# Kernel tuning notes

Hardware: AMD Instinct MI355X
Metric: run time of the kernel (lower is better)

## Reference

```python
import jax, jax.numpy as jnp
import numpy as np

STRIDES = (8, 16, 32, 64, 128)
SIZES = ((40, 40), (20, 20), (10, 10), (5, 5), (3, 3))
NUM_CLASSES = 80
SCORE_THR = 0.025
NMS_PRE = 1000
IOU_THR = 0.5
IMG = 320.0  # img_shape hardcoded to (320, 320); clamp uses max_shape[1]
B = 4


def setup_inputs() -> dict:
    key = jax.random.key(0)
    ks = jax.random.split(key, 15)
    inp = {}
    for i, (h, w) in enumerate(SIZES):
        inp[f"cls{i}"] = jax.random.normal(ks[3 * i], (B, NUM_CLASSES, h, w), dtype=jnp.float32)
        # bbox preds are ltrb distances; scale uniform noise to plausible pixel distances
        inp[f"bbox{i}"] = jax.random.uniform(ks[3 * i + 1], (B, 4, h, w), dtype=jnp.float32) * 64.0
        inp[f"ctr{i}"] = jax.random.normal(ks[3 * i + 2], (B, 1, h, w), dtype=jnp.float32)
    return inp


def _priors(h, w, stride):
    # MlvlPointGenerator: (arange + 0.5) * stride, x fastest-varying
    sx = (jnp.arange(w, dtype=jnp.float32) + 0.5) * stride
    sy = (jnp.arange(h, dtype=jnp.float32) + 0.5) * stride
    return jnp.stack([jnp.tile(sx, h), jnp.repeat(sy, w)], axis=-1)  # [h*w, 2]


def _distance2bbox(points, dist):
    x1 = points[:, 0] - dist[:, 0]
    y1 = points[:, 1] - dist[:, 1]
    x2 = points[:, 0] + dist[:, 2]
    y2 = points[:, 1] + dist[:, 3]
    # torch.clamp_ on the whole tensor: min=0, max=max_shape[1]=320
    return jnp.clip(jnp.stack([x1, y1, x2, y2], axis=-1), 0.0, IMG)


def _pairwise_iou(boxes):
    # torchvision-style IoU on [K,4] boxes
    area = (boxes[:, 2] - boxes[:, 0]) * (boxes[:, 3] - boxes[:, 1])
    lt = jnp.maximum(boxes[:, None, :2], boxes[None, :, :2])
    rb = jnp.minimum(boxes[:, None, 2:], boxes[None, :, 2:])
    wh = jnp.maximum(rb - lt, 0.0)
    inter = wh[..., 0] * wh[..., 1]
    union = area[:, None] + area[None, :] - inter
    safe = jnp.where(union > 0.0, union, 1.0)
    return jnp.where(union > 0.0, inter / safe, 0.0)


def _single(cls_l, bbox_l, ctr_l):
    """Post-process one image. Returns fixed-size (dets [K,5], labels [K], keep [K] bool)."""
    scores_l, labels_l, boxes_l, valid_l = [], [], [], []
    for lvl in range(5):
        h, w = SIZES[lvl]
        pri = _priors(h, w, STRIDES[lvl])
        s = jax.nn.sigmoid(jnp.transpose(cls_l[lvl], (1, 2, 0)).reshape(-1, NUM_CLASSES)).reshape(-1)
        bp = jnp.transpose(bbox_l[lvl], (1, 2, 0)).reshape(-1, 4)
        sf = jax.nn.sigmoid(jnp.transpose(ctr_l[lvl], (1, 2, 0)).reshape(-1))
        # filter_scores_and_topk: mask scores <= thr to -1 so they sort last; fixed-size top_k
        k = min(NMS_PRE, s.shape[0])
        top_s, top_i = jax.lax.top_k(jnp.where(s > SCORE_THR, s, -1.0), k)
        anchor = top_i // NUM_CLASSES
        label = top_i % NUM_CLASSES
        valid = top_s > SCORE_THR
        boxes = _distance2bbox(pri[anchor], bp[anchor])
        # scores multiplied by centerness score factor (FCOS)
        scores_l.append(jnp.where(valid, top_s * sf[anchor], -1.0))
        labels_l.append(label)
        boxes_l.append(boxes)
        valid_l.append(valid)
    scores = jnp.concatenate(scores_l)          # [K]
    labels = jnp.concatenate(labels_l)          # [K]
    boxes = jnp.concatenate(boxes_l, axis=0)    # [K,4]
    valid = jnp.concatenate(valid_l)            # [K]
    # sort by final score descending (NMS processes in score order)
    order = jnp.argsort(-scores)
    scores = scores[order]
    labels = labels[order]
    boxes = boxes[order]
    valid = valid[order]
    # batched_nms: per-class coordinate offset trick
    max_coord = boxes.max()
    off = boxes + (labels.astype(jnp.float32) * (max_coord + 1.0))[:, None]
    iou = _pairwise_iou(off)  # [K,K]
    K = scores.shape[0]
    idx = jnp.arange(K)

    def body(i, keep):
        sup = (iou[i] > IOU_THR) & (idx > i) & keep[i]
        return keep & jnp.logical_not(sup)

    keep = jax.lax.fori_loop(0, K, body, valid)
    dets = jnp.concatenate([boxes, scores[:, None]], axis=-1)  # [K,5]
    return dets, labels, keep


def reference(cls0, cls1, cls2, cls3, cls4, bbox0, bbox1, bbox2, bbox3, bbox4, ctr0, ctr1, ctr2, ctr3, ctr4):
    cls_l = (cls0, cls1, cls2, cls3, cls4)
    bbox_l = (bbox0, bbox1, bbox2, bbox3, bbox4)
    ctr_l = (ctr0, ctr1, ctr2, ctr3, ctr4)
    return jax.vmap(_single)(cls_l, bbox_l, ctr_l)
```

## Files before the change

### kernel.cpp

```cpp
#include <hip/hip_runtime.h>
#include <stdint.h>


#define BN 4
#define NC 80
#define TOT 170720
#define KTOT 4720
#define NWIN 74
#define NJT 19
#define TIE_CAP 4096
#define IMGSZ 320.0f
#define PAIR_CAP 131072
#define LDSP 12288
#define SPC_CAP 4096

struct InPtrs {
  const float* cls[5];
  const float* bbox[5];
  const float* ctr[5];
};

__device__ __forceinline__ uint32_t f2s(float f) {
  uint32_t x = __float_as_uint(f);
  return (x & 0x80000000u) ? ~x : (x | 0x80000000u);
}
__device__ __forceinline__ float s2f(uint32_t s) {
  uint32_t x = (s & 0x80000000u) ? (s & 0x7fffffffu) : ~s;
  return __uint_as_float(x);
}
__device__ __forceinline__ float sigmoid32(float v) {
  float e = (float)exp(-(double)v);
  return __fdiv_rn(1.0f, __fadd_rn(1.0f, e));
}
__device__ __forceinline__ void lvl_of(int e, int& l, int& le) {
  if (e < 128000)      { l = 0; le = e; }
  else if (e < 160000) { l = 1; le = e - 128000; }
  else if (e < 168000) { l = 2; le = e - 160000; }
  else if (e < 170000) { l = 3; le = e - 168000; }
  else                 { l = 4; le = e - 170000; }
}
__device__ __forceinline__ int kl_of(int l) {
  constexpr int KL[5] = {1000, 1000, 1000, 1000, 720};
  return KL[l];
}
__device__ __forceinline__ float clip32(float v) {
  return fminf(fmaxf(v, 0.0f), IMGSZ);
}
__device__ __forceinline__ void tile_of(int t, int& l, int& p0) {
  if (t < 25)       { l = 0; p0 = t * 64; }
  else if (t < 32)  { l = 1; p0 = (t - 25) * 64; }
  else if (t < 34)  { l = 2; p0 = (t - 32) * 64; }
  else if (t == 34) { l = 3; p0 = 0; }
  else              { l = 4; p0 = 0; }
}
__device__ __forceinline__ int iou_gt(float bx1, float by1, float bx2, float by2,
                                      float bai, float4 o) {
  float ta_ = __fmul_rn(__fsub_rn(o.z, o.x), __fsub_rn(o.w, o.y));
  float ltx = fmaxf(bx1, o.x), lty = fmaxf(by1, o.y);
  float rbx = fminf(bx2, o.z), rby = fminf(by2, o.w);
  float wd = fmaxf(__fsub_rn(rbx, ltx), 0.0f);
  float hg = fmaxf(__fsub_rn(rby, lty), 0.0f);
  float inter = __fmul_rn(wd, hg);
  float asum = __fadd_rn(bai, ta_);
  float uni  = __fsub_rn(asum, inter);
  float iou  = (uni > 0.0f) ? __fdiv_rn(inter, uni) : 0.0f;
  return (iou > 0.5f) ? 1 : 0;
}

__global__ void k_score(InPtrs in, uint32_t* __restrict__ su, uint32_t* __restrict__ hist0) {
  int b = blockIdx.y;
  int tl, p0; tile_of(blockIdx.x, tl, p0);
  constexpr int HWc[5]  = {1600, 400, 100, 25, 9};
  constexpr int LOFF[5] = {0, 128000, 160000, 168000, 170000};
  int hw = HWc[tl];
  int tw = min(64, hw - p0);
  int tid = threadIdx.x;
  __shared__ uint32_t lu[64 * 81];
  __shared__ uint32_t lh[1024];
  for (int i = tid; i < 1024; i += 256) lh[i] = 0;
  __syncthreads();
  int pf = tid & 63;
  if (pf < tw) {
    const float* cp = in.cls[tl] + (size_t)b * NC * hw + p0 + pf;
    for (int c = tid >> 6; c < NC; c += 4) {
      float v = cp[(size_t)c * hw];
      float s = sigmoid32(v);
      float m = (s > 0.025f) ? s : -1.0f;
      uint32_t u = f2s(m);
      lu[pf * 81 + c] = u;
      atomicAdd(&lh[u >> 22], 1u);
    }
  }
  __syncthreads();
  int bl = b * 5 + tl;
  for (int i = tid; i < 1024; i += 256)
    if (lh[i]) atomicAdd(&hist0[(size_t)bl * 1024 + i], lh[i]);
  int n = tw * NC;
  uint32_t* dst = su + (size_t)b * TOT + LOFF[tl] + p0 * NC;
  for (int idx = tid; idx < n; idx += 256)
    dst[idx] = lu[(idx / 80) * 81 + (idx % 80)];
}

__global__ void k_scan1(const uint32_t* __restrict__ su, const uint32_t* __restrict__ mpfx,
                        uint32_t* __restrict__ hist1) {
  int b = blockIdx.y;
  int tid = threadIdx.x;
  int e0 = blockIdx.x * 256;
  int e = e0 + tid;
  int l0, le0; lvl_of(e0, l0, le0);
  __shared__ uint32_t lh[2][1024];
  for (int i = tid; i < 2048; i += 256) lh[i >> 10][i & 1023] = 0;
  __syncthreads();
  if (e < TOT) {
    int l, le; lvl_of(e, l, le);
    uint32_t C = mpfx[b * 5 + l];
    uint32_t u = su[(size_t)b * TOT + e];
    if ((u >> 22) == (C >> 22)) atomicAdd(&lh[l - l0][(u >> 12) & 1023u], 1u);
  }
  __syncthreads();
  for (int s = 0; s < 2; s++) {
    int l = l0 + s;
    if (l >= 5) break;
    int bl = b * 5 + l;
    for (int i = tid; i < 1024; i += 256)
      if (lh[s][i]) atomicAdd(&hist1[(size_t)bl * 1024 + i], lh[s][i]);
  }
}

__global__ void k_scan2(const uint32_t* __restrict__ su, const uint32_t* __restrict__ mpfx,
                        uint32_t* __restrict__ hist2) {
  int b = blockIdx.y;
  int e = blockIdx.x * blockDim.x + threadIdx.x;
  if (e >= TOT) return;
  int l, le; lvl_of(e, l, le);
  int bl = b * 5 + l;
  uint32_t C = mpfx[bl];
  uint32_t u = su[(size_t)b * TOT + e];
  if ((u >> 12) == (C >> 12))
    atomicAdd(&hist2[(size_t)bl * 4096 + (u & 4095u)], 1u);
}

__global__ void k_findp(const uint32_t* __restrict__ hist, uint32_t* __restrict__ mpfx,
                        uint32_t* __restrict__ mk, int nbins, int shift, int pass) {
  int bl = blockIdx.x;
  uint32_t k = (pass == 0) ? (uint32_t)kl_of(bl % 5) : mk[bl];
  const uint32_t* h = hist + (size_t)bl * nbins;
  __shared__ uint32_t gsum[256];
  int tid = threadIdx.x;
  int per = nbins / 256;
  int base = tid * per;
  uint32_t s = 0;
  for (int i = 0; i < per; i++) s += h[base + i];
  gsum[tid] = s;
  __syncthreads();
  uint32_t above = 0;
  for (int t = tid + 1; t < 256; t++) above += gsum[t];
  if (above < k && above + s >= k) {
    uint32_t cum = above;
    for (int bin = base + per - 1; bin >= base; bin--) {
      uint32_t c = h[bin];
      if (cum < k && cum + c >= k) {
        uint32_t pfx = (pass == 0) ? 0u : mpfx[bl];
        mpfx[bl] = pfx | ((uint32_t)bin << shift);
        mk[bl] = k - cum;
        break;
      }
      cum += c;
    }
  }
}

__global__ void k_compact(const uint32_t* __restrict__ su, const uint32_t* __restrict__ mpfx,
                          uint32_t* __restrict__ selcnt, uint32_t* __restrict__ tiecnt,
                          uint32_t* __restrict__ selu, uint32_t* __restrict__ seli,
                          uint32_t* __restrict__ tiei) {
  int b = blockIdx.y;
  int tid = threadIdx.x;
  int e0 = blockIdx.x * 256;
  int e = e0 + tid;
  int l0, le0; lvl_of(e0, l0, le0);
  __shared__ uint32_t cnt[2], tcnt[2], gbase[2], tgbase[2];
  __shared__ uint32_t su_s[2][256], si_s[2][256];
  __shared__ uint32_t ti_s[2][256];
  if (tid < 2) { cnt[tid] = 0u; tcnt[tid] = 0u; }
  __syncthreads();
  if (e < TOT) {
    int l, le; lvl_of(e, l, le);
    int slot = l - l0;
    int bl = b * 5 + l;
    uint32_t u = su[(size_t)b * TOT + e];
    uint32_t C = mpfx[bl];
    if (u > C) {
      uint32_t p = atomicAdd(&cnt[slot], 1u);
      su_s[slot][p] = u;
      si_s[slot][p] = (uint32_t)le;
    } else if (u == C) {
      uint32_t p = atomicAdd(&tcnt[slot], 1u);
      ti_s[slot][p] = (uint32_t)le;
    }
  }
  __syncthreads();
  if (tid < 2) {
    int bl = b * 5 + l0 + tid;
    if (cnt[tid])  gbase[tid]  = atomicAdd(&selcnt[bl], cnt[tid]);
    if (tcnt[tid]) tgbase[tid] = atomicAdd(&tiecnt[bl], tcnt[tid]);
  }
  __syncthreads();
  for (int s = 0; s < 2; s++) {
    int bl = b * 5 + l0 + s;
    uint32_t n = cnt[s];
    for (uint32_t t = tid; t < n; t += 256) {
      uint32_t pos = gbase[s] + t;
      selu[(size_t)bl * 1024 + pos] = su_s[s][t];
      seli[(size_t)bl * 1024 + pos] = si_s[s][t];
    }
    uint32_t tn = tcnt[s];
    for (uint32_t t = tid; t < tn; t += 256) {
      uint32_t pos = tgbase[s] + t;
      if (pos < TIE_CAP) tiei[(size_t)bl * TIE_CAP + pos] = ti_s[s][t];
    }
  }
}

__global__ void k_ties(const uint32_t* __restrict__ mpfx, const uint32_t* __restrict__ mk,
                       const uint32_t* __restrict__ tiecnt, const uint32_t* __restrict__ tiei,
                       uint32_t* __restrict__ selu, uint32_t* __restrict__ seli) {
  int bl = blockIdx.x;
  int l = bl % 5;
  uint32_t C = mpfx[bl];
  uint32_t T = mk[bl];
  uint32_t G = (uint32_t)kl_of(l) - T;
  uint32_t Tc = tiecnt[bl];
  if (Tc > TIE_CAP) Tc = TIE_CAP;
  __shared__ uint32_t sh[TIE_CAP];
  for (uint32_t t = threadIdx.x; t < Tc; t += blockDim.x) sh[t] = tiei[(size_t)bl * TIE_CAP + t];
  __syncthreads();
  for (uint32_t t = threadIdx.x; t < Tc; t += blockDim.x) {
    uint32_t my = sh[t];
    uint32_t rank = 0;
    for (uint32_t q = 0; q < Tc; q++) rank += (sh[q] < my) ? 1u : 0u;
    if (rank < T) {
      selu[(size_t)bl * 1024 + G + rank] = C;
      seli[(size_t)bl * 1024 + G + rank] = my;
    }
  }
}

__global__ void k_emit(InPtrs in, const uint32_t* __restrict__ selu, const uint32_t* __restrict__ seli,
                       float* __restrict__ ccs, uint32_t* __restrict__ ccl,
                       uint32_t* __restrict__ ccv, float* __restrict__ ccb) {
  int bl = blockIdx.x;
  int chunk = blockIdx.y;
  int b = bl / 5, l = bl % 5;
  int k = kl_of(l);
  __shared__ uint64_t z[1024];
  int tid = threadIdx.x;
  for (int t = tid; t < 1024; t += 256) {
    if (t < k) {
      uint32_t u = selu[(size_t)bl * 1024 + t];
      uint32_t idx = seli[(size_t)bl * 1024 + t];
      z[t] = (((uint64_t)u) << 32) | (uint32_t)(~idx);
    } else z[t] = 0ull;
  }
  __syncthreads();
  int tg = chunk * 256 + tid;
  if (tg >= k) return;
  uint64_t zi = z[tg];
  uint32_t u = (uint32_t)(zi >> 32);
  uint32_t idx = ~(uint32_t)zi;
  int rank = 0;
  const uint4* z4 = (const uint4*)z;
  for (int j4 = 0; j4 < 512; j4++) {
    uint4 q = z4[j4];
    uint64_t za = (((uint64_t)q.y) << 32) | q.x;
    uint64_t zb = (((uint64_t)q.w) << 32) | q.z;
    rank += (za > zi) ? 1 : 0;
    rank += (zb > zi) ? 1 : 0;
  }
  constexpr int Wc[5]  = {40, 20, 10, 5, 3};
  constexpr int HWc[5] = {1600, 400, 100, 25, 9};
  constexpr float Sc[5] = {8.f, 16.f, 32.f, 64.f, 128.f};
  constexpr int COFF[5] = {0, 1000, 2000, 3000, 4000};
  int w = Wc[l], hw = HWc[l];
  float ms = s2f(u);
  int valid = (ms > 0.025f) ? 1 : 0;
  int p = (int)idx / NC, c = (int)idx % NC;
  int x = p % w, y = p / w;
  float sf = sigmoid32(in.ctr[l][(size_t)b * hw + p]);
  float score = valid ? __fmul_rn(ms, sf) : -1.0f;
  float px = __fmul_rn(__fadd_rn((float)x, 0.5f), Sc[l]);
  float py = __fmul_rn(__fadd_rn((float)y, 0.5f), Sc[l]);
  size_t bb = (size_t)b * 4 * hw;
  float d0 = in.bbox[l][bb + 0 * hw + p];
  float d1 = in.bbox[l][bb + 1 * hw + p];
  float d2 = in.bbox[l][bb + 2 * hw + p];
  float d3 = in.bbox[l][bb + 3 * hw + p];
  float x1 = clip32(__fsub_rn(px, d0)), y1 = clip32(__fsub_rn(py, d1));
  float x2 = clip32(__fadd_rn(px, d2)), y2 = clip32(__fadd_rn(py, d3));
  int o = b * KTOT + COFF[l] + rank;
  ccs[o] = score;
  ccl[o] = (uint32_t)c;
  ccv[o] = (uint32_t)valid;
  ccb[(size_t)o * 4 + 0] = x1; ccb[(size_t)o * 4 + 1] = y1;
  ccb[(size_t)o * 4 + 2] = x2; ccb[(size_t)o * 4 + 3] = y2;
}

__global__ void k_rank(const float* __restrict__ ccs, uint32_t* __restrict__ rankp) {
  int b = blockIdx.z;
  int jt = blockIdx.y;
  int ib = blockIdx.x;
  int tid = threadIdx.x;
  __shared__ uint32_t jk[256];
  int j0 = jt * 256;
  int jn = min(256, KTOT - j0);
  jk[tid] = (tid < jn) ? f2s(ccs[(size_t)b * KTOT + j0 + tid]) : 0u;
  __syncthreads();
  int e = ib * 256 + tid;
  if (e >= KTOT) return;
  uint32_t ke = f2s(ccs[(size_t)b * KTOT + e]);
  int rank = 0;
  const uint4* k4 = (const uint4*)jk;
#pragma unroll 8
  for (int q = 0; q < 64; q++) {
    uint4 kk = k4[q];
    int j = j0 + q * 4;
    rank += ((kk.x > ke) || (kk.x == ke && (j + 0) < e)) ? 1 : 0;
    rank += ((kk.y > ke) || (kk.y == ke && (j + 1) < e)) ? 1 : 0;
    rank += ((kk.z > ke) || (kk.z == ke && (j + 2) < e)) ? 1 : 0;
    rank += ((kk.w > ke) || (kk.w == ke && (j + 3) < e)) ? 1 : 0;
  }
  rankp[((size_t)b * NJT + jt) * KTOT + e] = (uint32_t)rank;
}

__global__ void k_scatter(const float* __restrict__ ccs, const uint32_t* __restrict__ ccl,
                          const uint32_t* __restrict__ ccv, const float* __restrict__ ccb,
                          const uint32_t* __restrict__ rankp,
                          float* __restrict__ ss, uint32_t* __restrict__ sl,
                          uint32_t* __restrict__ sv, float* __restrict__ sb,
                          uint32_t* __restrict__ maxcb) {
  int b = blockIdx.y;
  __shared__ float red[4];
  int tid = threadIdx.x;
  int e = blockIdx.x * 256 + tid;
  float mx = 0.0f;
  if (e < KTOT) {
    uint32_t rank = 0;
    for (int jt = 0; jt < NJT; jt++)
      rank += rankp[((size_t)b * NJT + jt) * KTOT + e];
    int sidx = b * KTOT + e;
    int d = b * KTOT + (int)rank;
    ss[d] = ccs[sidx];
    sl[d] = ccl[sidx];
    sv[d] = ccv[sidx];
    float b0 = ccb[(size_t)sidx * 4 + 0], b1 = ccb[(size_t)sidx * 4 + 1];
    float b2 = ccb[(size_t)sidx * 4 + 2], b3 = ccb[(size_t)sidx * 4 + 3];
    sb[(size_t)d * 4 + 0] = b0; sb[(size_t)d * 4 + 1] = b1;
    sb[(size_t)d * 4 + 2] = b2; sb[(size_t)d * 4 + 3] = b3;
    mx = fmaxf(fmaxf(b0, b1), fmaxf(b2, b3));
  }
  for (int o = 32; o; o >>= 1) mx = fmaxf(mx, __shfl_xor(mx, o));
  if ((tid & 63) == 0) red[tid >> 6] = mx;
  __syncthreads();
  if (tid == 0)
    atomicMax(&maxcb[b], __float_as_uint(fmaxf(fmaxf(red[0], red[1]), fmaxf(red[2], red[3]))));
}

__global__ void k_offbits(const float* __restrict__ sb, const uint32_t* __restrict__ sl,
                          const uint32_t* __restrict__ maxcb, const uint32_t* __restrict__ sv,
                          float* __restrict__ ob, unsigned long long* __restrict__ vbits,
                          uint32_t* __restrict__ paircnt,
                          uint32_t* __restrict__ clist, uint32_t* __restrict__ ccount) {
  int b = blockIdx.y;
  int tid = threadIdx.x;
  if (blockIdx.x == 0 && b == 0 && tid < BN) paircnt[tid] = 0u;
  int e = blockIdx.x * 256 + tid;
  int pred = 0;
  if (e < KTOT) {
    int r = b * KTOT + e;
    float scale = __fadd_rn(__uint_as_float(maxcb[b]), 1.0f);
    uint32_t c = sl[r];
    float offv = __fmul_rn((float)c, scale);
    float x1 = __fadd_rn(sb[(size_t)r * 4 + 0], offv);
    float y1 = __fadd_rn(sb[(size_t)r * 4 + 1], offv);
    float x2 = __fadd_rn(sb[(size_t)r * 4 + 2], offv);
    float y2 = __fadd_rn(sb[(size_t)r * 4 + 3], offv);
    ob[(size_t)r * 4 + 0] = x1; ob[(size_t)r * 4 + 1] = y1;
    ob[(size_t)r * 4 + 2] = x2; ob[(size_t)r * 4 + 3] = y2;
    pred = (sv[r] != 0u);
    uint32_t pos = atomicAdd(&ccount[b * NC + c], 1u);
    clist[((size_t)b * NC + c) * KTOT + pos] = (uint32_t)e;
  }
  unsigned long long m = __ballot(pred);
  int w = blockIdx.x * 4 + (tid >> 6);
  if ((tid & 63) == 0 && w < NWIN) vbits[b * NWIN + w] = m;
}

__global__ void k_pairs(const uint32_t* __restrict__ clist, const uint32_t* __restrict__ ccount,
                        const float* __restrict__ ob,
                        uint32_t* __restrict__ pairs, uint32_t* __restrict__ paircnt) {
  int b = blockIdx.y;
  int c = blockIdx.x;
  int m = (int)ccount[b * NC + c];
  if (m < 2) return;
  int tid = threadIdx.x;
  const uint32_t* cl = clist + ((size_t)b * NC + c) * KTOT;
  const float4* ob4 = (const float4*)ob + (size_t)b * KTOT;
  __shared__ uint32_t lst[KTOT];
  __shared__ uint32_t spc[SPC_CAP];
  __shared__ float4 tb[256];
  __shared__ uint32_t jidx[256];
  __shared__ uint32_t scnt, sbase;
  for (int t = tid; t < m; t += 256) lst[t] = cl[t];
  if (tid == 0) scnt = 0u;
  for (int jt = 0; jt < m; jt += 256) {
    int jn = min(256, m - jt);
    __syncthreads();
    if (tid < jn) { uint32_t gj = lst[jt + tid]; jidx[tid] = gj; tb[tid] = ob4[gj]; }
    __syncthreads();
    for (int i = tid; i < m; i += 256) {
      uint32_t gi = lst[i];
      float4 v = ob4[gi];
      float bai = __fmul_rn(__fsub_rn(v.z, v.x), __fsub_rn(v.w, v.y));
      for (int jj = 0; jj < jn; jj++) {
        uint32_t gj = jidx[jj];
        if (gj > gi && iou_gt(v.x, v.y, v.z, v.w, bai, tb[jj])) {
          uint32_t pos = atomicAdd(&scnt, 1u);
          if (pos < SPC_CAP) spc[pos] = (gi << 13) | gj;
        }
      }
    }
  }
  __syncthreads();
  uint32_t total = scnt;
  if (total == 0u) return;
  if (tid == 0) sbase = atomicAdd(&paircnt[b], total);
  __syncthreads();
  uint32_t gb = sbase;
  uint32_t* gp = pairs + (size_t)b * PAIR_CAP;
  if (total <= (uint32_t)SPC_CAP) {
    for (uint32_t t = tid; t < total; t += 256)
      if (gb + t < PAIR_CAP) gp[gb + t] = spc[t];
  } else {
    if (tid == 0) scnt = 0u;
    for (int jt = 0; jt < m; jt += 256) {
      int jn = min(256, m - jt);
      __syncthreads();
      if (tid < jn) { uint32_t gj = lst[jt + tid]; jidx[tid] = gj; tb[tid] = ob4[gj]; }
      __syncthreads();
      for (int i = tid; i < m; i += 256) {
        uint32_t gi = lst[i];
        float4 v = ob4[gi];
        float bai = __fmul_rn(__fsub_rn(v.z, v.x), __fsub_rn(v.w, v.y));
        for (int jj = 0; jj < jn; jj++) {
          uint32_t gj = jidx[jj];
          if (gj > gi && iou_gt(v.x, v.y, v.z, v.w, bai, tb[jj])) {
            uint32_t pos = gb + atomicAdd(&scnt, 1u);
            if (pos < PAIR_CAP) gp[pos] = (gi << 13) | gj;
          }
        }
      }
    }
  }
}

__global__ void k_nms(const float* __restrict__ ob,
                      const unsigned long long* __restrict__ vbits,
                      unsigned long long* __restrict__ keepw,
                      const uint32_t* __restrict__ pairs,
                      const uint32_t* __restrict__ paircnt) {
  int b = blockIdx.x;
  int tid = threadIdx.x;
  int lane = tid & 63;
  __shared__ unsigned long long tdl[NWIN * 64];
  __shared__ unsigned long long svl[NWIN];
  __shared__ unsigned long long sup[NWIN];
  __shared__ unsigned long long kwsh;
  __shared__ uint32_t plp[LDSP];
  __shared__ uint32_t wstart[NWIN + 1];
  __shared__ uint32_t wtmp[NWIN];
  for (int i = tid; i < NWIN * 64; i += 256) tdl[i] = 0ull;
  if (tid < NWIN) { svl[tid] = vbits[b * NWIN + tid]; sup[tid] = 0ull; wtmp[tid] = 0u; }
  uint32_t npairs = paircnt[b];
  bool useP = (npairs <= (uint32_t)PAIR_CAP);
  bool useL = (npairs <= (uint32_t)LDSP);
  const uint32_t* gpl = pairs + (size_t)b * PAIR_CAP;
  __syncthreads();
  unsigned int* sup32 = (unsigned int*)sup;
  unsigned int* tdl32 = (unsigned int*)tdl;
  if (useP) {
    for (uint32_t t = tid; t < npairs; t += 256) {
      uint32_t p = gpl[t];
      int i = (int)(p >> 13), j = (int)(p & 8191u);
      if ((i >> 6) == (j >> 6)) {
        int r = ((i >> 6) * 64 + (i & 63)) * 2 + ((j & 63) >> 5);
        atomicOr(&tdl32[r], 1u << (j & 31));
      } else {
        atomicAdd(&wtmp[i >> 6], 1u);
      }
    }
    __syncthreads();
    if (tid == 0) {
      uint32_t acc = 0;
      for (int w = 0; w < NWIN; w++) { wstart[w] = acc; acc += wtmp[w]; }
      wstart[NWIN] = acc;
    }
    __syncthreads();
    if (tid < NWIN) wtmp[tid] = 0u;
    __syncthreads();
    if (useL) {
      for (uint32_t t = tid; t < npairs; t += 256) {
        uint32_t p = gpl[t];
        int i = (int)(p >> 13), j = (int)(p & 8191u);
        if ((i >> 6) == (j >> 6)) continue;
        uint32_t w = (uint32_t)(i >> 6);
        uint32_t pos = wstart[w] + atomicAdd(&wtmp[w], 1u);
        plp[pos] = p;
      }
    }
    __syncthreads();
    if (tid < 64) {
      for (int w = 0; w < NWIN; w++) {
        unsigned long long row = tdl[w * 64 + lane];
        unsigned long long m = __ballot(row != 0ull);
        unsigned long long sa = sup[w];
        unsigned long long sval = svl[w];
        unsigned int rlo = (unsigned int)row, rhi = (unsigned int)(row >> 32);
        while (m) {
          int i = __ffsll((long long)m) - 1;
          m &= m - 1;
          if (((sval >> i) & 1ull) && !((sa >> i) & 1ull)) {
            unsigned int lo = (unsigned int)__builtin_amdgcn_readlane((int)rlo, i);
            unsigned int hi = (unsigned int)__builtin_amdgcn_readlane((int)rhi, i);
            sa |= (((unsigned long long)hi) << 32) | (unsigned long long)lo;
          }
        }
        unsigned long long kw = sval & ~sa;
        if (lane == 0) keepw[b * NWIN + w] = kw;
        if (useL) {
          for (uint32_t t = wstart[w] + lane; t < wstart[w + 1]; t += 64) {
            uint32_t p = plp[t];
            int i = (int)(p >> 13);
            if (!((kw >> (i & 63)) & 1ull)) continue;
            int j = (int)(p & 8191u);
            atomicOr(&sup32[j >> 5], 1u << (j & 31));
          }
        } else {
          for (uint32_t t = lane; t < npairs; t += 64) {
            uint32_t p = gpl[t];
            int i = (int)(p >> 13);
            if ((i >> 6) != w) continue;
            int j = (int)(p & 8191u);
            if ((j >> 6) == w) continue;
            if (!((kw >> (i & 63)) & 1ull)) continue;
            atomicOr(&sup32[j >> 5], 1u << (j & 31));
          }
        }
        __threadfence_block();
      }
    }
  } else {
    int wv = tid >> 6;
    const float4* ob4 = (const float4*)ob + (size_t)b * KTOT;
    for (int w = 0; w < NWIN; w++) {
      if (wv == 0) {
        int i = w * 64 + lane;
        unsigned long long row = 0ull;
        if (i < KTOT) {
          float4 v = ob4[i];
          float bai = __fmul_rn(__fsub_rn(v.z, v.x), __fsub_rn(v.w, v.y));
          for (int jj = 0; jj < 64; jj++) {
            int j = w * 64 + jj;
            if (j > i && j < KTOT)
              row |= ((unsigned long long)iou_gt(v.x, v.y, v.z, v.w, bai, ob4[j])) << jj;
          }
        }
        unsigned long long m = __ballot(row != 0ull);
        unsigned long long sa = sup[w];
        unsigned long long sval = svl[w];
        unsigned int rlo = (unsigned int)row, rhi = (unsigned int)(row >> 32);
        while (m) {
          int i2 = __ffsll((long long)m) - 1;
          m &= m - 1;
          if (((sval >> i2) & 1ull) && !((sa >> i2) & 1ull)) {
            unsigned int lo = (unsigned int)__builtin_amdgcn_readlane((int)rlo, i2);
            unsigned int hi = (unsigned int)__builtin_amdgcn_readlane((int)rhi, i2);
            sa |= (((unsigned long long)hi) << 32) | (unsigned long long)lo;
          }
        }
        unsigned long long kw = sval & ~sa;
        if (lane == 0) { keepw[b * NWIN + w] = kw; kwsh = kw; }
      }
      __syncthreads();
      unsigned long long kw = kwsh;
      for (int ii = 0; ii < 64; ii++) {
        if (!((kw >> ii) & 1ull)) continue;
        int i = w * 64 + ii;
        if (i >= KTOT) break;
        float4 v = ob4[i];
        float bai = __fmul_rn(__fsub_rn(v.z, v.x), __fsub_rn(v.w, v.y));
        for (int j = (w + 1) * 64 + tid; j < KTOT; j += 256)
          if (iou_gt(v.x, v.y, v.z, v.w, bai, ob4[j]))
            atomicOr(&sup32[j >> 5], 1u << (j & 31));
      }
      __syncthreads();
    }
  }
}

__global__ void k_out(const float* __restrict__ ss, const uint32_t* __restrict__ sl,
                      const float* __restrict__ sb, const unsigned long long* __restrict__ keepw,
                      float* __restrict__ out) {
  int r = blockIdx.x * blockDim.x + threadIdx.x;
  if (r >= BN * KTOT) return;
  int b = r / KTOT;
  int e = r - b * KTOT;
  unsigned int kp = (unsigned int)((keepw[b * NWIN + (e >> 6)] >> (e & 63)) & 1ull);
  out[(size_t)r * 5 + 0] = sb[(size_t)r * 4 + 0];
  out[(size_t)r * 5 + 1] = sb[(size_t)r * 4 + 1];
  out[(size_t)r * 5 + 2] = sb[(size_t)r * 4 + 2];
  out[(size_t)r * 5 + 3] = sb[(size_t)r * 4 + 3];
  out[(size_t)r * 5 + 4] = ss[r];
  out[(size_t)BN * KTOT * 5 + r] = (float)sl[r];
  out[(size_t)BN * KTOT * 6 + r] = kp ? 1.0f : 0.0f;
}

extern "C" void kernel_launch(void* const* d_in, const int* in_sizes, int n_in,
                              void* d_out, int out_size, void* d_ws, size_t ws_size,
                              hipStream_t stream) {
  InPtrs ip;
  for (int l = 0; l < 5; l++) {
    ip.cls[l]  = (const float*)d_in[3 * l + 0];
    ip.bbox[l] = (const float*)d_in[3 * l + 1];
    ip.ctr[l]  = (const float*)d_in[3 * l + 2];
  }

  size_t off = 0;
  auto alloc = [&](size_t n) {
    char* p = (char*)d_ws + off;
    off = (off + n + 255) & ~(size_t)255;
    return p;
  };
  const size_t SU_BYTES   = (size_t)BN * TOT * 4;
  const size_t HIST_BYTES = (20ull * 1024 + 20ull * 1024 + 20ull * 4096) * 4;
  const size_t EXTRA      = 2048;
  char* r0p = (char*)alloc(((SU_BYTES + 255) & ~(size_t)255) + HIST_BYTES + EXTRA);
  uint32_t* su    = (uint32_t*)r0p;
  uint32_t* hist0 = (uint32_t*)(r0p + ((SU_BYTES + 255) & ~(size_t)255));
  uint32_t* hist1 = hist0 + 20ull * 1024;
  uint32_t* hist2 = hist1 + 20ull * 1024;
  uint32_t* selcnt = hist2 + 20ull * 4096;
  uint32_t* tiecnt = selcnt + 20;
  uint32_t* maxcb  = tiecnt + 20;
  uint32_t* ccount = maxcb + BN;

  uint32_t* mpfx   = (uint32_t*)alloc(20 * 4);
  uint32_t* mk     = (uint32_t*)alloc(20 * 4);
  uint32_t* selu   = (uint32_t*)alloc(20ull * 1024 * 4);
  uint32_t* seli   = (uint32_t*)alloc(20ull * 1024 * 4);
  uint32_t* tiei   = (uint32_t*)alloc(20ull * TIE_CAP * 4);
  float*    ccs    = (float*)   alloc((size_t)BN * KTOT * 4);
  uint32_t* ccl    = (uint32_t*)alloc((size_t)BN * KTOT * 4);
  uint32_t* ccv    = (uint32_t*)alloc((size_t)BN * KTOT * 4);
  float*    ccb    = (float*)   alloc((size_t)BN * KTOT * 16);
  float*    ss     = (float*)   alloc((size_t)BN * KTOT * 4);
  uint32_t* sl     = (uint32_t*)alloc((size_t)BN * KTOT * 4);
  uint32_t* sv     = (uint32_t*)alloc((size_t)BN * KTOT * 4);
  float*    sb     = (float*)   alloc((size_t)BN * KTOT * 16);
  float*    ob     = (float*)   alloc((size_t)BN * KTOT * 16);
  uint32_t* rankp  = (uint32_t*)alloc((size_t)BN * NJT * KTOT * 4);
  uint32_t* clist  = (uint32_t*)alloc((size_t)BN * NC * KTOT * 4);
  unsigned long long* vbits = (unsigned long long*)alloc((size_t)BN * NWIN * 8);
  unsigned long long* keepw = (unsigned long long*)alloc((size_t)BN * NWIN * 8);
  uint32_t* pairs   = (uint32_t*)alloc((size_t)BN * PAIR_CAP * 4);
  uint32_t* paircnt = (uint32_t*)alloc(BN * 4);
  (void)ws_size; (void)in_sizes; (void)n_in; (void)out_size;

  dim3 gscan((TOT + 255) / 256, BN);
  hipMemsetAsync(hist0, 0, HIST_BYTES + EXTRA, stream);
  k_score<<<dim3(36, BN), 256, 0, stream>>>(ip, su, hist0);
  k_findp<<<20, 256, 0, stream>>>(hist0, mpfx, mk, 1024, 22, 0);
  k_scan1<<<gscan, 256, 0, stream>>>(su, mpfx, hist1);
  k_findp<<<20, 256, 0, stream>>>(hist1, mpfx, mk, 1024, 12, 1);
  k_scan2<<<gscan, 256, 0, stream>>>(su, mpfx, hist2);
  k_findp<<<20, 256, 0, stream>>>(hist2, mpfx, mk, 4096, 0, 2);
  k_compact<<<gscan, 256, 0, stream>>>(su, mpfx, selcnt, tiecnt, selu, seli, tiei);
  k_ties<<<20, 256, 0, stream>>>(mpfx, mk, tiecnt, tiei, selu, seli);
  k_emit<<<dim3(20, 4), 256, 0, stream>>>(ip, selu, seli, ccs, ccl, ccv, ccb);
  k_rank<<<dim3(19, NJT, BN), 256, 0, stream>>>(ccs, rankp);
  k_scatter<<<dim3(19, BN), 256, 0, stream>>>(ccs, ccl, ccv, ccb, rankp, ss, sl, sv, sb, maxcb);
  k_offbits<<<dim3(19, BN), 256, 0, stream>>>(sb, sl, maxcb, sv, ob, vbits, paircnt, clist, ccount);
  k_pairs<<<dim3(NC, BN), 256, 0, stream>>>(clist, ccount, ob, pairs, paircnt);
  k_nms<<<BN, 256, 0, stream>>>(ob, vbits, keepw, pairs, paircnt);
  k_out<<<(BN * KTOT + 255) / 256, 256, 0, stream>>>(ss, sl, sb, keepw, (float*)d_out);
}
```

Before: 240.9 us.

## Drop third radix pass via tie ranking and fuse output write into NMS

The third radix-select pass (scan over 4096 low bits plus a findp launch) is removed. Compaction now stops at the 20-bit prefix and stores the full key for tied elements, and the tie kernel ranks them by key and then by index. The separate output kernel is folded into the tail of the NMS kernel, which keeps keep-bits in shared memory. This cuts two launches plus a full scan, and a third launch and a global round trip for the keep words. The trade-off is a larger O(T²) tie-ranking set if many keys share a 20-bit prefix, and an output write done by only 4 blocks.

```diff
diff --git a/kernel.cpp b/kernel.cpp
--- a/kernel.cpp
+++ b/kernel.cpp
@@ -127,19 +127,6 @@
   }
 }
 
-__global__ void k_scan2(const uint32_t* __restrict__ su, const uint32_t* __restrict__ mpfx,
-                        uint32_t* __restrict__ hist2) {
-  int b = blockIdx.y;
-  int e = blockIdx.x * blockDim.x + threadIdx.x;
-  if (e >= TOT) return;
-  int l, le; lvl_of(e, l, le);
-  int bl = b * 5 + l;
-  uint32_t C = mpfx[bl];
-  uint32_t u = su[(size_t)b * TOT + e];
-  if ((u >> 12) == (C >> 12))
-    atomicAdd(&hist2[(size_t)bl * 4096 + (u & 4095u)], 1u);
-}
-
 __global__ void k_findp(const uint32_t* __restrict__ hist, uint32_t* __restrict__ mpfx,
                         uint32_t* __restrict__ mk, int nbins, int shift, int pass) {
   int bl = blockIdx.x;
@@ -173,7 +160,7 @@
 __global__ void k_compact(const uint32_t* __restrict__ su, const uint32_t* __restrict__ mpfx,
                           uint32_t* __restrict__ selcnt, uint32_t* __restrict__ tiecnt,
                           uint32_t* __restrict__ selu, uint32_t* __restrict__ seli,
-                          uint32_t* __restrict__ tiei) {
+                          uint32_t* __restrict__ tiei, uint32_t* __restrict__ tieu) {
   int b = blockIdx.y;
   int tid = threadIdx.x;
   int e0 = blockIdx.x * 256;
@@ -181,7 +168,7 @@
   int l0, le0; lvl_of(e0, l0, le0);
   __shared__ uint32_t cnt[2], tcnt[2], gbase[2], tgbase[2];
   __shared__ uint32_t su_s[2][256], si_s[2][256];
-  __shared__ uint32_t ti_s[2][256];
+  __shared__ uint32_t ti_s[2][256], tu_s[2][256];
   if (tid < 2) { cnt[tid] = 0u; tcnt[tid] = 0u; }
   __syncthreads();
   if (e < TOT) {
@@ -189,14 +176,16 @@
     int slot = l - l0;
     int bl = b * 5 + l;
     uint32_t u = su[(size_t)b * TOT + e];
-    uint32_t C = mpfx[bl];
-    if (u > C) {
+    uint32_t C20 = mpfx[bl] >> 12;
+    uint32_t u20 = u >> 12;
+    if (u20 > C20) {
       uint32_t p = atomicAdd(&cnt[slot], 1u);
       su_s[slot][p] = u;
       si_s[slot][p] = (uint32_t)le;
-    } else if (u == C) {
+    } else if (u20 == C20) {
       uint32_t p = atomicAdd(&tcnt[slot], 1u);
       ti_s[slot][p] = (uint32_t)le;
+      tu_s[slot][p] = u;
     }
   }
   __syncthreads();
@@ -217,31 +206,39 @@
     uint32_t tn = tcnt[s];
     for (uint32_t t = tid; t < tn; t += 256) {
       uint32_t pos = tgbase[s] + t;
-      if (pos < TIE_CAP) tiei[(size_t)bl * TIE_CAP + pos] = ti_s[s][t];
-    }
-  }
-}
-
-__global__ void k_ties(const uint32_t* __restrict__ mpfx, const uint32_t* __restrict__ mk,
+      if (pos < TIE_CAP) {
+        tiei[(size_t)bl * TIE_CAP + pos] = ti_s[s][t];
+        tieu[(size_t)bl * TIE_CAP + pos] = tu_s[s][t];
+      }
+    }
+  }
+}
+
+__global__ void k_ties(const uint32_t* __restrict__ mk,
                        const uint32_t* __restrict__ tiecnt, const uint32_t* __restrict__ tiei,
+                       const uint32_t* __restrict__ tieu,
                        uint32_t* __restrict__ selu, uint32_t* __restrict__ seli) {
   int bl = blockIdx.x;
   int l = bl % 5;
-  uint32_t C = mpfx[bl];
   uint32_t T = mk[bl];
   uint32_t G = (uint32_t)kl_of(l) - T;
   uint32_t Tc = tiecnt[bl];
   if (Tc > TIE_CAP) Tc = TIE_CAP;
-  __shared__ uint32_t sh[TIE_CAP];
-  for (uint32_t t = threadIdx.x; t < Tc; t += blockDim.x) sh[t] = tiei[(size_t)bl * TIE_CAP + t];
-  __syncthreads();
+  __shared__ uint32_t shi[TIE_CAP];
+  __shared__ uint32_t shu[TIE_CAP];
   for (uint32_t t = threadIdx.x; t < Tc; t += blockDim.x) {
-    uint32_t my = sh[t];
+    shi[t] = tiei[(size_t)bl * TIE_CAP + t];
+    shu[t] = tieu[(size_t)bl * TIE_CAP + t];
+  }
+  __syncthreads();
+  for (uint32_t t = threadIdx.x; t < Tc; t += blockDim.x) {
+    uint32_t mu = shu[t], mi = shi[t];
     uint32_t rank = 0;
-    for (uint32_t q = 0; q < Tc; q++) rank += (sh[q] < my) ? 1u : 0u;
+    for (uint32_t q = 0; q < Tc; q++)
+      rank += ((shu[q] > mu) || (shu[q] == mu && shi[q] < mi)) ? 1u : 0u;
     if (rank < T) {
-      selu[(size_t)bl * 1024 + G + rank] = C;
-      seli[(size_t)bl * 1024 + G + rank] = my;
+      selu[(size_t)bl * 1024 + G + rank] = mu;
+      seli[(size_t)bl * 1024 + G + rank] = mi;
     }
   }
 }
@@ -465,15 +462,18 @@
 
 __global__ void k_nms(const float* __restrict__ ob,
                       const unsigned long long* __restrict__ vbits,
-                      unsigned long long* __restrict__ keepw,
+                      const float* __restrict__ ss, const uint32_t* __restrict__ sl,
+                      const float* __restrict__ sb,
                       const uint32_t* __restrict__ pairs,
-                      const uint32_t* __restrict__ paircnt) {
+                      const uint32_t* __restrict__ paircnt,
+                      float* __restrict__ out) {
   int b = blockIdx.x;
   int tid = threadIdx.x;
   int lane = tid & 63;
   __shared__ unsigned long long tdl[NWIN * 64];
   __shared__ unsigned long long svl[NWIN];
   __shared__ unsigned long long sup[NWIN];
+  __shared__ unsigned long long kws[NWIN];
   __shared__ unsigned long long kwsh;
   __shared__ uint32_t plp[LDSP];
   __shared__ uint32_t wstart[NWIN + 1];
@@ -535,7 +535,7 @@
           }
         }
         unsigned long long kw = sval & ~sa;
-        if (lane == 0) keepw[b * NWIN + w] = kw;
+        if (lane == 0) kws[w] = kw;
         if (useL) {
           for (uint32_t t = wstart[w] + lane; t < wstart[w + 1]; t += 64) {
             uint32_t p = plp[t];
@@ -588,7 +588,7 @@
           }
         }
         unsigned long long kw = sval & ~sa;
-        if (lane == 0) { keepw[b * NWIN + w] = kw; kwsh = kw; }
+        if (lane == 0) { kws[w] = kw; kwsh = kw; }
       }
       __syncthreads();
       unsigned long long kw = kwsh;
@@ -605,23 +605,18 @@
       __syncthreads();
     }
   }
-}
-
-__global__ void k_out(const float* __restrict__ ss, const uint32_t* __restrict__ sl,
-                      const float* __restrict__ sb, const unsigned long long* __restrict__ keepw,
-                      float* __restrict__ out) {
-  int r = blockIdx.x * blockDim.x + threadIdx.x;
-  if (r >= BN * KTOT) return;
-  int b = r / KTOT;
-  int e = r - b * KTOT;
-  unsigned int kp = (unsigned int)((keepw[b * NWIN + (e >> 6)] >> (e & 63)) & 1ull);
-  out[(size_t)r * 5 + 0] = sb[(size_t)r * 4 + 0];
-  out[(size_t)r * 5 + 1] = sb[(size_t)r * 4 + 1];
-  out[(size_t)r * 5 + 2] = sb[(size_t)r * 4 + 2];
-  out[(size_t)r * 5 + 3] = sb[(size_t)r * 4 + 3];
-  out[(size_t)r * 5 + 4] = ss[r];
-  out[(size_t)BN * KTOT * 5 + r] = (float)sl[r];
-  out[(size_t)BN * KTOT * 6 + r] = kp ? 1.0f : 0.0f;
+  __syncthreads();
+  for (int e = tid; e < KTOT; e += 256) {
+    int r = b * KTOT + e;
+    unsigned int kp = (unsigned int)((kws[e >> 6] >> (e & 63)) & 1ull);
+    out[(size_t)r * 5 + 0] = sb[(size_t)r * 4 + 0];
+    out[(size_t)r * 5 + 1] = sb[(size_t)r * 4 + 1];
+    out[(size_t)r * 5 + 2] = sb[(size_t)r * 4 + 2];
+    out[(size_t)r * 5 + 3] = sb[(size_t)r * 4 + 3];
+    out[(size_t)r * 5 + 4] = ss[r];
+    out[(size_t)BN * KTOT * 5 + r] = (float)sl[r];
+    out[(size_t)BN * KTOT * 6 + r] = kp ? 1.0f : 0.0f;
+  }
 }
 
 extern "C" void kernel_launch(void* const* d_in, const int* in_sizes, int n_in,
@@ -641,14 +636,13 @@
     return p;
   };
   const size_t SU_BYTES   = (size_t)BN * TOT * 4;
-  const size_t HIST_BYTES = (20ull * 1024 + 20ull * 1024 + 20ull * 4096) * 4;
+  const size_t HIST_BYTES = (20ull * 1024 + 20ull * 1024) * 4;
   const size_t EXTRA      = 2048;
   char* r0p = (char*)alloc(((SU_BYTES + 255) & ~(size_t)255) + HIST_BYTES + EXTRA);
   uint32_t* su    = (uint32_t*)r0p;
   uint32_t* hist0 = (uint32_t*)(r0p + ((SU_BYTES + 255) & ~(size_t)255));
   uint32_t* hist1 = hist0 + 20ull * 1024;
-  uint32_t* hist2 = hist1 + 20ull * 1024;
-  uint32_t* selcnt = hist2 + 20ull * 4096;
+  uint32_t* selcnt = hist1 + 20ull * 1024;
   uint32_t* tiecnt = selcnt + 20;
   uint32_t* maxcb  = tiecnt + 20;
   uint32_t* ccount = maxcb + BN;
@@ -658,6 +652,7 @@
   uint32_t* selu   = (uint32_t*)alloc(20ull * 1024 * 4);
   uint32_t* seli   = (uint32_t*)alloc(20ull * 1024 * 4);
   uint32_t* tiei   = (uint32_t*)alloc(20ull * TIE_CAP * 4);
+  uint32_t* tieu   = (uint32_t*)alloc(20ull * TIE_CAP * 4);
   float*    ccs    = (float*)   alloc((size_t)BN * KTOT * 4);
   uint32_t* ccl    = (uint32_t*)alloc((size_t)BN * KTOT * 4);
   uint32_t* ccv    = (uint32_t*)alloc((size_t)BN * KTOT * 4);
@@ -670,7 +665,6 @@
   uint32_t* rankp  = (uint32_t*)alloc((size_t)BN * NJT * KTOT * 4);
   uint32_t* clist  = (uint32_t*)alloc((size_t)BN * NC * KTOT * 4);
   unsigned long long* vbits = (unsigned long long*)alloc((size_t)BN * NWIN * 8);
-  unsigned long long* keepw = (unsigned long long*)alloc((size_t)BN * NWIN * 8);
   uint32_t* pairs   = (uint32_t*)alloc((size_t)BN * PAIR_CAP * 4);
   uint32_t* paircnt = (uint32_t*)alloc(BN * 4);
   (void)ws_size; (void)in_sizes; (void)n_in; (void)out_size;
@@ -681,15 +675,12 @@
   k_findp<<<20, 256, 0, stream>>>(hist0, mpfx, mk, 1024, 22, 0);
   k_scan1<<<gscan, 256, 0, stream>>>(su, mpfx, hist1);
   k_findp<<<20, 256, 0, stream>>>(hist1, mpfx, mk, 1024, 12, 1);
-  k_scan2<<<gscan, 256, 0, stream>>>(su, mpfx, hist2);
-  k_findp<<<20, 256, 0, stream>>>(hist2, mpfx, mk, 4096, 0, 2);
-  k_compact<<<gscan, 256, 0, stream>>>(su, mpfx, selcnt, tiecnt, selu, seli, tiei);
-  k_ties<<<20, 256, 0, stream>>>(mpfx, mk, tiecnt, tiei, selu, seli);
+  k_compact<<<gscan, 256, 0, stream>>>(su, mpfx, selcnt, tiecnt, selu, seli, tiei, tieu);
+  k_ties<<<20, 256, 0, stream>>>(mk, tiecnt, tiei, tieu, selu, seli);
   k_emit<<<dim3(20, 4), 256, 0, stream>>>(ip, selu, seli, ccs, ccl, ccv, ccb);
   k_rank<<<dim3(19, NJT, BN), 256, 0, stream>>>(ccs, rankp);
   k_scatter<<<dim3(19, BN), 256, 0, stream>>>(ccs, ccl, ccv, ccb, rankp, ss, sl, sv, sb, maxcb);
   k_offbits<<<dim3(19, BN), 256, 0, stream>>>(sb, sl, maxcb, sv, ob, vbits, paircnt, clist, ccount);
   k_pairs<<<dim3(NC, BN), 256, 0, stream>>>(clist, ccount, ob, pairs, paircnt);
-  k_nms<<<BN, 256, 0, stream>>>(ob, vbits, keepw, pairs, paircnt);
-  k_out<<<(BN * KTOT + 255) / 256, 256, 0, stream>>>(ss, sl, sb, keepw, (float*)d_out);
-}
+  k_nms<<<BN, 256, 0, stream>>>(ob, vbits, ss, sl, sb, pairs, paircnt, (float*)d_out);
+}
```

Result: no change. 238.7 us (-0.9%).
